# Optimization experiments

Measured on AMD Instinct MI355X. Metric: run time of the kernel, lower is better.

## Reference

```python
import jax, jax.numpy as jnp
import numpy as np

B, T, E = 4, 2048, 1024
H = 16
DH = E // H
SCALE = DH ** -0.5


def setup_inputs() -> dict:
    key = jax.random.key(0)
    ks = jax.random.split(key, 5)
    # small init scale for weights to keep softmax well-conditioned
    return {
        "x": jax.random.normal(ks[0], (B, T, E), dtype=jnp.float32),
        "w_qkv": jax.random.normal(ks[1], (3 * E, E), dtype=jnp.float32) * 0.02,
        "b_qkv": jax.random.normal(ks[2], (3 * E,), dtype=jnp.float32) * 0.02,
        "w_proj": jax.random.normal(ks[3], (E, E), dtype=jnp.float32) * 0.02,
        "b_proj": jax.random.normal(ks[4], (E,), dtype=jnp.float32) * 0.02,
    }


def reference(x, w_qkv, b_qkv, w_proj, b_proj):
    Bs, Ts, Es = x.shape
    # fused qkv projection (torch Linear: y = x W^T + b)
    qkv = x @ w_qkv.T + b_qkv                       # [B,T,3E]
    qkv = qkv.reshape(Bs, Ts, 3, H, DH)
    q, k, v = qkv[:, :, 0], qkv[:, :, 1], qkv[:, :, 2]  # [B,T,H,DH]
    # scores: materialize full TxT matrix per head, as in the original
    scores = jnp.einsum("bthd,bshd->bhts", q, k) * SCALE  # [B,H,T,T]
    causal = jnp.tril(jnp.ones((Ts, Ts), dtype=bool))
    scores = jnp.where(causal[None, None], scores, jnp.float32(-jnp.inf))
    attn = jax.nn.softmax(scores, axis=-1)
    # dropout = 0.0 (eval / deterministic reference)
    out = jnp.einsum("bhts,bshd->bthd", attn, v)    # [B,T,H,DH]
    out = out.reshape(Bs, Ts, Es)
    return out @ w_proj.T + b_proj
```

## Files before the change

### kernel.cpp

```cpp
#include <hip/hip_runtime.h>
#include <hip/hip_bf16.h>

#define B_ 4
#define T_ 2048
#define E_ 1024
#define H_ 16
#define DH_ 64
#define QSCALE_ 0.18033688f

typedef __attribute__((ext_vector_type(8))) short bf16x8;
typedef __attribute__((ext_vector_type(4))) float f32x4;
typedef unsigned int u32;

__device__ inline ushort f2bf(float f) {
    union { float f; unsigned u; } v; v.f = f;
    unsigned r = (v.u + 0x7fffu + ((v.u >> 16) & 1u)) >> 16;
    return (ushort)r;
}

__device__ inline u32 pack2bf(float a, float b) {
    union { float f; u32 u; } ua, ub; ua.f = a; ub.f = b;
    return __builtin_amdgcn_perm(ub.u, ua.u, 0x07060302);
}

__device__ inline void gload16(const ushort* g, ushort* l) {
    __builtin_amdgcn_global_load_lds((const __attribute__((address_space(1))) u32*)g,
                                     (__attribute__((address_space(3))) u32*)l, 16, 0, 0);
}

__global__ void cvt_all(const float* __restrict__ x, const float* __restrict__ wq,
                        const float* __restrict__ wp,
                        ushort* __restrict__ xo, ushort* __restrict__ wqo, ushort* __restrict__ wpo)
{
    const int NX = B_ * T_ * E_ / 4;
    const int NW = 3 * E_ * E_ / 4;
    int i = blockIdx.x * 256 + threadIdx.x;
    const float* s; ushort* d; int off;
    if (i < NX)            { s = x;  d = xo;  off = i; }
    else if (i < NX + NW)  { s = wq; d = wqo; off = i - NX; }
    else                   { s = wp; d = wpo; off = i - NX - NW; }
    float4 f = ((const float4*)s)[off];
    ushort4 u;
    u.x = f2bf(f.x); u.y = f2bf(f.y); u.z = f2bf(f.z); u.w = f2bf(f.w);
    ((ushort4*)d)[off] = u;
}


#define STAGE3(t_) { const int ss_ = (t_) & 3; const int sk_ = (t_) * 32;      \
    gload16(gA0 + sk_, &As[ss_][wave * 512]);                                  \
    gload16(gA1 + sk_, &As[ss_][4096 + wave * 512]);                           \
    gload16(gB0 + sk_, &Bs[ss_][wave * 512]); }

#define GPHASE(t_, vmstr_, DOSTAGE_, ...) do {                                 \
    const int seg_ = (t_) & 3;                                                 \
    bf16x8 afr[4], bfr[4];                                                     \
    _Pragma("unroll") for (int i_ = 0; i_ < 4; i_++)                           \
        afr[i_] = *(const bf16x8*)&As[seg_][(mbase + i_ * 16) * 32 + rofs];    \
    _Pragma("unroll") for (int j_ = 0; j_ < 4; j_++)                           \
        bfr[j_] = *(const bf16x8*)&Bs[seg_][(nbase + j_ * 16) * 32 + rofs];    \
    if (DOSTAGE_) STAGE3((t_) + 3);                                            \
    asm volatile("s_waitcnt " vmstr_ ::: "memory");                            \
    __builtin_amdgcn_s_barrier();                                              \
    asm volatile("s_waitcnt lgkmcnt(0)" ::: "memory");                         \
    __builtin_amdgcn_sched_barrier(0);                                         \
    __builtin_amdgcn_s_setprio(1);                                             \
    __VA_ARGS__                                                                \
    __builtin_amdgcn_s_setprio(0);                                             \
    __builtin_amdgcn_sched_barrier(0);                                         \
    __builtin_amdgcn_s_barrier();                                              \
    __builtin_amdgcn_sched_barrier(0);                                         \
} while (0)

#define MFMA_QKV                                                               \
    if (ct) {                                                                  \
        _Pragma("unroll") for (int i_ = 0; i_ < 4; i_++)                       \
        _Pragma("unroll") for (int j_ = 0; j_ < 4; j_++)                       \
            acc[i_][j_] = __builtin_amdgcn_mfma_f32_16x16x32_bf16(bfr[j_], afr[i_], acc[i_][j_], 0, 0, 0); \
    } else {                                                                   \
        _Pragma("unroll") for (int i_ = 0; i_ < 4; i_++)                       \
        _Pragma("unroll") for (int j_ = 0; j_ < 4; j_++)                       \
            acc[i_][j_] = __builtin_amdgcn_mfma_f32_16x16x32_bf16(afr[i_], bfr[j_], acc[i_][j_], 0, 0, 0); \
    }

#define MFMA_CT                                                                \
    _Pragma("unroll") for (int i_ = 0; i_ < 4; i_++)                           \
    _Pragma("unroll") for (int j_ = 0; j_ < 4; j_++)                           \
        acc[i_][j_] = __builtin_amdgcn_mfma_f32_16x16x32_bf16(bfr[j_], afr[i_], acc[i_][j_], 0, 0, 0);

__global__ __launch_bounds__(512, 2) void gemm_qkv(
    const ushort* __restrict__ Xb, const ushort* __restrict__ Wb,
    const float* __restrict__ bias,
    ushort* __restrict__ Q, ushort* __restrict__ K, ushort* __restrict__ Vt)
{
    __shared__ ushort As[4][256 * 32];
    __shared__ ushort Bs[4][128 * 32];
    const int m0 = blockIdx.x * 256;
    const int n0 = blockIdx.y * 128;
    const int kind = n0 >> 10;
    const int tid  = threadIdx.x;
    const int wave = tid >> 6, lane = tid & 63;
    const int lrow = lane & 15, quad = lane >> 4;
    const int mbase = (wave >> 1) * 64;
    const int nbase = (wave & 1) * 64;
    const int rofs = (lrow >> 1) * 64 + (((((lrow & 1) << 2) | quad) ^ (lrow >> 1)) * 8);
    const int sx  = (lane & 7) ^ (lane >> 3);
    const int sRl = 2 * (lane >> 3) + (sx >> 2);
    const int su  = (sx & 3) * 8;

    const ushort* gA0 = Xb + (size_t)(m0 + wave * 16 + sRl) * 1024 + su;
    const ushort* gA1 = gA0 + (size_t)128 * 1024;
    const ushort* gB0 = Wb + (size_t)(n0 + wave * 16 + sRl) * 1024 + su;

    const int b = m0 >> 11;
    const bool ct = (kind != 2);

    f32x4 acc[4][4];
#pragma unroll
    for (int i = 0; i < 4; i++)
#pragma unroll
        for (int j = 0; j < 4; j++) acc[i][j] = f32x4{0.f, 0.f, 0.f, 0.f};

    STAGE3(0); STAGE3(1); STAGE3(2);
    asm volatile("s_waitcnt vmcnt(6)" ::: "memory");
    __builtin_amdgcn_s_barrier();
    __builtin_amdgcn_sched_barrier(0);

#pragma unroll 4
    for (int t = 0; t < 29; t++) GPHASE(t, "vmcnt(6)", 1, MFMA_QKV);
    GPHASE(29, "vmcnt(3)", 0, MFMA_QKV);
    GPHASE(30, "vmcnt(0)", 0, MFMA_QKV);
    GPHASE(31, "vmcnt(0)", 0, MFMA_QKV);

    if (ct) {
        ushort* dst = (kind == 0) ? Q : K;
        const float scale = (kind == 0) ? QSCALE_ : 1.f;
#pragma unroll
        for (int j = 0; j < 4; j++) {
            int nq = (n0 & 1023) + nbase + j * 16 + quad * 4;
            int h = nq >> 6, d = nq & 63;
            float4 bv = *(const float4*)&bias[n0 + nbase + j * 16 + quad * 4];
            size_t bh = (size_t)(b * H_ + h);
#pragma unroll
            for (int i = 0; i < 4; i++) {
                int t = (m0 + mbase + i * 16 + lrow) & 2047;
                ushort4 o;
                o.x = f2bf((acc[i][j][0] + bv.x) * scale);
                o.y = f2bf((acc[i][j][1] + bv.y) * scale);
                o.z = f2bf((acc[i][j][2] + bv.z) * scale);
                o.w = f2bf((acc[i][j][3] + bv.w) * scale);
                *(ushort4*)&dst[(bh * T_ + t) * DH_ + d] = o;
            }
        }
    } else {
#pragma unroll
        for (int j = 0; j < 4; j++) {
            int nv = (n0 & 1023) + nbase + j * 16 + lrow;
            int h = nv >> 6, d = nv & 63;
            float bv = bias[n0 + nbase + j * 16 + lrow];
            size_t bh = (size_t)(b * H_ + h);
#pragma unroll
            for (int i = 0; i < 4; i++) {
                int t = (m0 + mbase + i * 16 + quad * 4) & 2047;
                ushort4 o;
                o.x = f2bf(acc[i][j][0] + bv);
                o.y = f2bf(acc[i][j][1] + bv);
                o.z = f2bf(acc[i][j][2] + bv);
                o.w = f2bf(acc[i][j][3] + bv);
                *(ushort4*)&Vt[(bh * DH_ + d) * T_ + t] = o;
            }
        }
    }
}

#define LDT_ 76

__global__ __launch_bounds__(256) void flash_attn(
    const ushort* __restrict__ Q, const ushort* __restrict__ K,
    const ushort* __restrict__ Vg,
    ushort* __restrict__ O)
{
    __shared__ ushort Ks[64 * LDT_];
    __shared__ ushort Vt[64 * LDT_];
    __shared__ ushort Ps[128 * LDT_];

    const int qtA = 15 - blockIdx.x;
    const int qtB = blockIdx.x;
    const int bh = blockIdx.y;
    const int tid  = threadIdx.x;
    const int wave = tid >> 6, lane = tid & 63;
    const int lrow = lane & 15, quad = lane >> 4;
    const int sr = tid >> 2, sc = (tid & 3) * 16;

    const ushort* Qbh = Q  + (size_t)bh * T_ * DH_;
    const ushort* Kbh = K  + (size_t)bh * T_ * DH_;
    const ushort* Vbh = Vg + (size_t)bh * DH_ * T_;
    const int b_ = bh >> 4, h_ = bh & 15;

    auto stageQ = [&](int qt, bf16x8 qa[2][2]) {
        int qr = tid >> 1, qc = (tid & 1) * 32;
        const ushort* src = &Qbh[(size_t)(qt * 128 + qr) * DH_ + qc];
#pragma unroll
        for (int i = 0; i < 4; i++)
            *(int4*)&Ps[qr * LDT_ + qc + 8 * i] = *(const int4*)&src[8 * i];
        __syncthreads();
#pragma unroll
        for (int s = 0; s < 2; s++)
#pragma unroll
            for (int h = 0; h < 2; h++)
                qa[s][h] = *(const bf16x8*)&Ps[(s * 64 + wave * 16 + lrow) * LDT_ + h * 32 + quad * 8];
    };

    bf16x8 qaA[2][2], qaB[2][2];
    stageQ(qtA, qaA);
    __syncthreads();
    stageQ(qtB, qaB);

    auto run = [&](const bf16x8 (&qa)[2][2], int qt) {
        const int lastkt = 2 * qt + 1;

        int4 kr0 = *(const int4*)&Kbh[(size_t)sr * DH_ + sc];
        int4 kr1 = *(const int4*)&Kbh[(size_t)sr * DH_ + sc + 8];
        int4 vr0 = *(const int4*)&Vbh[(size_t)sr * T_ + sc];
        int4 vr1 = *(const int4*)&Vbh[(size_t)sr * T_ + sc + 8];

        float ls[2] = {0.f, 0.f};
        f32x4 accO[2][4];
#pragma unroll
        for (int s = 0; s < 2; s++)
#pragma unroll
            for (int j = 0; j < 4; j++) accO[s][j] = f32x4{0.f, 0.f, 0.f, 0.f};

        for (int kt = 0; kt <= lastkt; ++kt) {
            __syncthreads();
            *(int4*)&Ks[sr * LDT_ + sc]     = kr0;
            *(int4*)&Ks[sr * LDT_ + sc + 8] = kr1;
            *(int4*)&Vt[sr * LDT_ + sc]     = vr0;
            *(int4*)&Vt[sr * LDT_ + sc + 8] = vr1;
            __syncthreads();
            if (kt < lastkt) {
                kr0 = *(const int4*)&Kbh[(size_t)((kt + 1) * 64 + sr) * DH_ + sc];
                kr1 = *(const int4*)&Kbh[(size_t)((kt + 1) * 64 + sr) * DH_ + sc + 8];
                vr0 = *(const int4*)&Vbh[(size_t)sr * T_ + (kt + 1) * 64 + sc];
                vr1 = *(const int4*)&Vbh[(size_t)sr * T_ + (kt + 1) * 64 + sc + 8];
            }

            bf16x8 kb0[4], kb1[4];
#pragma unroll
            for (int j = 0; j < 4; j++) {
                kb0[j] = *(const bf16x8*)&Ks[(j * 16 + lrow) * LDT_ + quad * 8];
                kb1[j] = *(const bf16x8*)&Ks[(j * 16 + lrow) * LDT_ + 32 + quad * 8];
            }

            const bool do0 = (kt != lastkt);
#pragma unroll
            for (int s = 0; s < 2; s++) {
                if (s == 0 && !do0) continue;
                f32x4 st[4];
#pragma unroll
                for (int j = 0; j < 4; j++) {
                    f32x4 sj = f32x4{0.f, 0.f, 0.f, 0.f};
                    sj = __builtin_amdgcn_mfma_f32_16x16x32_bf16(kb0[j], qa[s][0], sj, 0, 0, 0);
                    sj = __builtin_amdgcn_mfma_f32_16x16x32_bf16(kb1[j], qa[s][1], sj, 0, 0, 0);
                    st[j] = sj;
                }
                if (kt == 2 * qt + s) {
                    const int qrow = qt * 128 + s * 64 + wave * 16 + lrow;
                    const int keyb = kt * 64 + quad * 4;
#pragma unroll
                    for (int j = 0; j < 4; j++)
#pragma unroll
                        for (int r = 0; r < 4; r++)
                            if (keyb + j * 16 + r > qrow) st[j][r] = -1e30f;
                }
                float lp = 0.f;
#pragma unroll
                for (int j = 0; j < 4; j++)
#pragma unroll
                    for (int r = 0; r < 4; r++) {
                        float p = __builtin_amdgcn_exp2f(st[j][r]);
                        st[j][r] = p;
                        lp += p;
                    }
                ls[s] += lp;
                ushort* prow = &Ps[(s * 64 + wave * 16 + lrow) * LDT_ + quad * 4];
#pragma unroll
                for (int j = 0; j < 4; j++) {
                    *(u32*)&prow[j * 16]     = pack2bf(st[j][0], st[j][1]);
                    *(u32*)&prow[j * 16 + 2] = pack2bf(st[j][2], st[j][3]);
                }
            }

            bf16x8 vb0[4], vb1[4];
#pragma unroll
            for (int j = 0; j < 4; j++) {
                vb0[j] = *(const bf16x8*)&Vt[(j * 16 + lrow) * LDT_ + quad * 8];
                vb1[j] = *(const bf16x8*)&Vt[(j * 16 + lrow) * LDT_ + 32 + quad * 8];
            }
#pragma unroll
            for (int s = 0; s < 2; s++) {
                if (s == 0 && !do0) continue;
                bf16x8 pa0 = *(const bf16x8*)&Ps[(s * 64 + wave * 16 + lrow) * LDT_ + quad * 8];
                bf16x8 pa1 = *(const bf16x8*)&Ps[(s * 64 + wave * 16 + lrow) * LDT_ + 32 + quad * 8];
#pragma unroll
                for (int jd = 0; jd < 4; jd++) {
                    accO[s][jd] = __builtin_amdgcn_mfma_f32_16x16x32_bf16(pa0, vb0[jd], accO[s][jd], 0, 0, 0);
                    accO[s][jd] = __builtin_amdgcn_mfma_f32_16x16x32_bf16(pa1, vb1[jd], accO[s][jd], 0, 0, 0);
                }
            }
        }

#pragma unroll
        for (int s = 0; s < 2; s++) {
            ls[s] += __shfl_xor(ls[s], 16, 64);
            ls[s] += __shfl_xor(ls[s], 32, 64);
        }
#pragma unroll
        for (int s = 0; s < 2; s++) {
#pragma unroll
            for (int r = 0; r < 4; r++) {
                float lv = __shfl(ls[s], quad * 4 + r, 64);
                float inv = 1.f / lv;
                int t = qt * 128 + s * 64 + wave * 16 + quad * 4 + r;
#pragma unroll
                for (int jd = 0; jd < 4; jd++) {
                    int d = jd * 16 + lrow;
                    O[((size_t)(b_ * T_ + t)) * E_ + h_ * DH_ + d] = f2bf(accO[s][jd][r] * inv);
                }
            }
        }
    };

    run(qaA, qtA);
    run(qaB, qtB);
}

__global__ __launch_bounds__(512, 2) void gemm_proj(
    const ushort* __restrict__ Ob, const ushort* __restrict__ Wb,
    const float* __restrict__ bias, float* __restrict__ out)
{
    __shared__ ushort As[4][256 * 32];
    __shared__ ushort Bs[4][128 * 32];
    const int m0 = blockIdx.x * 256;
    const int n0 = blockIdx.y * 128;
    const int tid  = threadIdx.x;
    const int wave = tid >> 6, lane = tid & 63;
    const int lrow = lane & 15, quad = lane >> 4;
    const int mbase = (wave >> 1) * 64;
    const int nbase = (wave & 1) * 64;
    const int rofs = (lrow >> 1) * 64 + (((((lrow & 1) << 2) | quad) ^ (lrow >> 1)) * 8);
    const int sx  = (lane & 7) ^ (lane >> 3);
    const int sRl = 2 * (lane >> 3) + (sx >> 2);
    const int su  = (sx & 3) * 8;

    const ushort* gA0 = Ob + (size_t)(m0 + wave * 16 + sRl) * 1024 + su;
    const ushort* gA1 = gA0 + (size_t)128 * 1024;
    const ushort* gB0 = Wb + (size_t)(n0 + wave * 16 + sRl) * 1024 + su;

    f32x4 acc[4][4];
#pragma unroll
    for (int i = 0; i < 4; i++)
#pragma unroll
        for (int j = 0; j < 4; j++) acc[i][j] = f32x4{0.f, 0.f, 0.f, 0.f};

    STAGE3(0); STAGE3(1); STAGE3(2);
    asm volatile("s_waitcnt vmcnt(6)" ::: "memory");
    __builtin_amdgcn_s_barrier();
    __builtin_amdgcn_sched_barrier(0);

#pragma unroll 4
    for (int t = 0; t < 29; t++) GPHASE(t, "vmcnt(6)", 1, MFMA_CT);
    GPHASE(29, "vmcnt(3)", 0, MFMA_CT);
    GPHASE(30, "vmcnt(0)", 0, MFMA_CT);
    GPHASE(31, "vmcnt(0)", 0, MFMA_CT);

#pragma unroll
    for (int j = 0; j < 4; j++) {
        int n = n0 + nbase + j * 16 + quad * 4;
        float4 bv = *(const float4*)&bias[n];
#pragma unroll
        for (int i = 0; i < 4; i++) {
            int m = m0 + mbase + i * 16 + lrow;
            float4 o;
            o.x = acc[i][j][0] + bv.x;
            o.y = acc[i][j][1] + bv.y;
            o.z = acc[i][j][2] + bv.z;
            o.w = acc[i][j][3] + bv.w;
            *(float4*)&out[(size_t)m * 1024 + n] = o;
        }
    }
}

extern "C" void kernel_launch(void* const* d_in, const int* in_sizes, int n_in,
                              void* d_out, int out_size, void* d_ws, size_t ws_size,
                              hipStream_t stream) {
    const float* x      = (const float*)d_in[0];
    const float* w_qkv  = (const float*)d_in[1];
    const float* b_qkv  = (const float*)d_in[2];
    const float* w_proj = (const float*)d_in[3];
    const float* b_proj = (const float*)d_in[4];
    float* out = (float*)d_out;

    char* ws = (char*)d_ws;
    ushort* Xb     = (ushort*)ws; ws += (size_t)B_ * T_ * E_ * 2;
    ushort* Wqkvb  = (ushort*)ws; ws += (size_t)3 * E_ * E_ * 2;
    ushort* Wprojb = (ushort*)ws; ws += (size_t)E_ * E_ * 2;
    ushort* Qb     = (ushort*)ws; ws += (size_t)B_ * H_ * T_ * DH_ * 2;
    ushort* Kb     = (ushort*)ws; ws += (size_t)B_ * H_ * T_ * DH_ * 2;
    ushort* Vtb    = (ushort*)ws; ws += (size_t)B_ * H_ * T_ * DH_ * 2;
    ushort* Ob     = (ushort*)ws; ws += (size_t)B_ * T_ * E_ * 2;

    int ntot = (B_ * T_ * E_ + 3 * E_ * E_ + E_ * E_) / 4;
    cvt_all<<<ntot / 256, 256, 0, stream>>>(x, w_qkv, w_proj, Xb, Wqkvb, Wprojb);

    gemm_qkv<<<dim3(32, 24), 512, 0, stream>>>(Xb, Wqkvb, b_qkv, Qb, Kb, Vtb);
    flash_attn<<<dim3(8, 64), 256, 0, stream>>>(Qb, Kb, Vtb, Ob);
    gemm_proj<<<dim3(32, 8), 512, 0, stream>>>(Ob, Wprojb, b_proj, out);
}
```

Measured before the change: 251.6 us.

## Use 4-wave GEMM blocks with 128x64 warp tiles and 3-stage LDS ring

```diff
diff --git a/kernel.cpp b/kernel.cpp
--- a/kernel.cpp
+++ b/kernel.cpp
@@ -46,19 +46,21 @@
 }
 
 
-#define STAGE3(t_) { const int ss_ = (t_) & 3; const int sk_ = (t_) * 32;      \
-    gload16(gA0 + sk_, &As[ss_][wave * 512]);                                  \
-    gload16(gA1 + sk_, &As[ss_][4096 + wave * 512]);                           \
-    gload16(gB0 + sk_, &Bs[ss_][wave * 512]); }
-
-#define GPHASE(t_, vmstr_, DOSTAGE_, ...) do {                                 \
-    const int seg_ = (t_) & 3;                                                 \
-    bf16x8 afr[4], bfr[4];                                                     \
-    _Pragma("unroll") for (int i_ = 0; i_ < 4; i_++)                           \
-        afr[i_] = *(const bf16x8*)&As[seg_][(mbase + i_ * 16) * 32 + rofs];    \
+#define STAGE6(ss_, t_) { const int sk_ = (t_) * 32;                           \
+    gload16(gA0 + sk_,             &As[ss_][(wave * 4 + 0) * 512]);            \
+    gload16(gA0 + 16 * 1024 + sk_, &As[ss_][(wave * 4 + 1) * 512]);            \
+    gload16(gA0 + 32 * 1024 + sk_, &As[ss_][(wave * 4 + 2) * 512]);            \
+    gload16(gA0 + 48 * 1024 + sk_, &As[ss_][(wave * 4 + 3) * 512]);            \
+    gload16(gB0 + sk_,             &Bs[ss_][(wave * 2 + 0) * 512]);            \
+    gload16(gB0 + 16 * 1024 + sk_, &Bs[ss_][(wave * 2 + 1) * 512]); }
+
+#define GPHASE(segC_, segS_, t_, vmstr_, DOSTAGE_, ...) do {                   \
+    bf16x8 afr[8], bfr[4];                                                     \
+    _Pragma("unroll") for (int i_ = 0; i_ < 8; i_++)                           \
+        afr[i_] = *(const bf16x8*)&As[segC_][(mbase + i_ * 16) * 32 + rofs];   \
     _Pragma("unroll") for (int j_ = 0; j_ < 4; j_++)                           \
-        bfr[j_] = *(const bf16x8*)&Bs[seg_][(nbase + j_ * 16) * 32 + rofs];    \
-    if (DOSTAGE_) STAGE3((t_) + 3);                                            \
+        bfr[j_] = *(const bf16x8*)&Bs[segC_][(nbase + j_ * 16) * 32 + rofs];   \
+    if (DOSTAGE_) STAGE6(segS_, (t_) + 2);                                     \
     asm volatile("s_waitcnt " vmstr_ ::: "memory");                            \
     __builtin_amdgcn_s_barrier();                                              \
     asm volatile("s_waitcnt lgkmcnt(0)" ::: "memory");                         \
@@ -73,63 +75,67 @@
 
 #define MFMA_QKV                                                               \
     if (ct) {                                                                  \
-        _Pragma("unroll") for (int i_ = 0; i_ < 4; i_++)                       \
+        _Pragma("unroll") for (int i_ = 0; i_ < 8; i_++)                       \
         _Pragma("unroll") for (int j_ = 0; j_ < 4; j_++)                       \
             acc[i_][j_] = __builtin_amdgcn_mfma_f32_16x16x32_bf16(bfr[j_], afr[i_], acc[i_][j_], 0, 0, 0); \
     } else {                                                                   \
-        _Pragma("unroll") for (int i_ = 0; i_ < 4; i_++)                       \
+        _Pragma("unroll") for (int i_ = 0; i_ < 8; i_++)                       \
         _Pragma("unroll") for (int j_ = 0; j_ < 4; j_++)                       \
             acc[i_][j_] = __builtin_amdgcn_mfma_f32_16x16x32_bf16(afr[i_], bfr[j_], acc[i_][j_], 0, 0, 0); \
     }
 
 #define MFMA_CT                                                                \
-    _Pragma("unroll") for (int i_ = 0; i_ < 4; i_++)                           \
+    _Pragma("unroll") for (int i_ = 0; i_ < 8; i_++)                           \
     _Pragma("unroll") for (int j_ = 0; j_ < 4; j_++)                           \
         acc[i_][j_] = __builtin_amdgcn_mfma_f32_16x16x32_bf16(bfr[j_], afr[i_], acc[i_][j_], 0, 0, 0);
 
-__global__ __launch_bounds__(512, 2) void gemm_qkv(
+#define GEMM_MAIN(MFMABLK_)                                                    \
+    STAGE6(0, 0); STAGE6(1, 1);                                                \
+    asm volatile("s_waitcnt vmcnt(6)" ::: "memory");                           \
+    __builtin_amdgcn_s_barrier();                                              \
+    __builtin_amdgcn_sched_barrier(0);                                         \
+    _Pragma("unroll 1")                                                        \
+    for (int t = 0; t < 30; t += 3) {                                          \
+        GPHASE(0, 2, t + 0, "vmcnt(6)", 1, MFMABLK_);                          \
+        GPHASE(1, 0, t + 1, "vmcnt(6)", 1, MFMABLK_);                          \
+        GPHASE(2, 1, t + 2, "vmcnt(6)", 1, MFMABLK_);                          \
+    }                                                                          \
+    GPHASE(0, 0, 30, "vmcnt(0)", 0, MFMABLK_);                                 \
+    GPHASE(1, 0, 31, "vmcnt(0)", 0, MFMABLK_);
+
+__global__ __launch_bounds__(256, 2) void gemm_qkv(
     const ushort* __restrict__ Xb, const ushort* __restrict__ Wb,
     const float* __restrict__ bias,
     ushort* __restrict__ Q, ushort* __restrict__ K, ushort* __restrict__ Vt)
 {
-    __shared__ ushort As[4][256 * 32];
-    __shared__ ushort Bs[4][128 * 32];
+    __shared__ ushort As[3][256 * 32];
+    __shared__ ushort Bs[3][128 * 32];
     const int m0 = blockIdx.x * 256;
     const int n0 = blockIdx.y * 128;
     const int kind = n0 >> 10;
     const int tid  = threadIdx.x;
     const int wave = tid >> 6, lane = tid & 63;
     const int lrow = lane & 15, quad = lane >> 4;
-    const int mbase = (wave >> 1) * 64;
+    const int mbase = (wave >> 1) * 128;
     const int nbase = (wave & 1) * 64;
     const int rofs = (lrow >> 1) * 64 + (((((lrow & 1) << 2) | quad) ^ (lrow >> 1)) * 8);
     const int sx  = (lane & 7) ^ (lane >> 3);
     const int sRl = 2 * (lane >> 3) + (sx >> 2);
     const int su  = (sx & 3) * 8;
 
-    const ushort* gA0 = Xb + (size_t)(m0 + wave * 16 + sRl) * 1024 + su;
-    const ushort* gA1 = gA0 + (size_t)128 * 1024;
-    const ushort* gB0 = Wb + (size_t)(n0 + wave * 16 + sRl) * 1024 + su;
+    const ushort* gA0 = Xb + (size_t)(m0 + wave * 64 + sRl) * 1024 + su;
+    const ushort* gB0 = Wb + (size_t)(n0 + wave * 32 + sRl) * 1024 + su;
 
     const int b = m0 >> 11;
     const bool ct = (kind != 2);
 
-    f32x4 acc[4][4];
-#pragma unroll
-    for (int i = 0; i < 4; i++)
+    f32x4 acc[8][4];
+#pragma unroll
+    for (int i = 0; i < 8; i++)
 #pragma unroll
         for (int j = 0; j < 4; j++) acc[i][j] = f32x4{0.f, 0.f, 0.f, 0.f};
 
-    STAGE3(0); STAGE3(1); STAGE3(2);
-    asm volatile("s_waitcnt vmcnt(6)" ::: "memory");
-    __builtin_amdgcn_s_barrier();
-    __builtin_amdgcn_sched_barrier(0);
-
-#pragma unroll 4
-    for (int t = 0; t < 29; t++) GPHASE(t, "vmcnt(6)", 1, MFMA_QKV);
-    GPHASE(29, "vmcnt(3)", 0, MFMA_QKV);
-    GPHASE(30, "vmcnt(0)", 0, MFMA_QKV);
-    GPHASE(31, "vmcnt(0)", 0, MFMA_QKV);
+    GEMM_MAIN(MFMA_QKV)
 
     if (ct) {
         ushort* dst = (kind == 0) ? Q : K;
@@ -141,7 +147,7 @@
             float4 bv = *(const float4*)&bias[n0 + nbase + j * 16 + quad * 4];
             size_t bh = (size_t)(b * H_ + h);
 #pragma unroll
-            for (int i = 0; i < 4; i++) {
+            for (int i = 0; i < 8; i++) {
                 int t = (m0 + mbase + i * 16 + lrow) & 2047;
                 ushort4 o;
                 o.x = f2bf((acc[i][j][0] + bv.x) * scale);
@@ -159,7 +165,7 @@
             float bv = bias[n0 + nbase + j * 16 + lrow];
             size_t bh = (size_t)(b * H_ + h);
 #pragma unroll
-            for (int i = 0; i < 4; i++) {
+            for (int i = 0; i < 8; i++) {
                 int t = (m0 + mbase + i * 16 + quad * 4) & 2047;
                 ushort4 o;
                 o.x = f2bf(acc[i][j][0] + bv);
@@ -334,51 +340,41 @@
     run(qaB, qtB);
 }
 
-__global__ __launch_bounds__(512, 2) void gemm_proj(
+__global__ __launch_bounds__(256, 2) void gemm_proj(
     const ushort* __restrict__ Ob, const ushort* __restrict__ Wb,
     const float* __restrict__ bias, float* __restrict__ out)
 {
-    __shared__ ushort As[4][256 * 32];
-    __shared__ ushort Bs[4][128 * 32];
+    __shared__ ushort As[3][256 * 32];
+    __shared__ ushort Bs[3][128 * 32];
     const int m0 = blockIdx.x * 256;
     const int n0 = blockIdx.y * 128;
     const int tid  = threadIdx.x;
     const int wave = tid >> 6, lane = tid & 63;
     const int lrow = lane & 15, quad = lane >> 4;
-    const int mbase = (wave >> 1) * 64;
+    const int mbase = (wave >> 1) * 128;
     const int nbase = (wave & 1) * 64;
     const int rofs = (lrow >> 1) * 64 + (((((lrow & 1) << 2) | quad) ^ (lrow >> 1)) * 8);
     const int sx  = (lane & 7) ^ (lane >> 3);
     const int sRl = 2 * (lane >> 3) + (sx >> 2);
     const int su  = (sx & 3) * 8;
 
-    const ushort* gA0 = Ob + (size_t)(m0 + wave * 16 + sRl) * 1024 + su;
-    const ushort* gA1 = gA0 + (size_t)128 * 1024;
-    const ushort* gB0 = Wb + (size_t)(n0 + wave * 16 + sRl) * 1024 + su;
-
-    f32x4 acc[4][4];
-#pragma unroll
-    for (int i = 0; i < 4; i++)
+    const ushort* gA0 = Ob + (size_t)(m0 + wave * 64 + sRl) * 1024 + su;
+    const ushort* gB0 = Wb + (size_t)(n0 + wave * 32 + sRl) * 1024 + su;
+
+    f32x4 acc[8][4];
+#pragma unroll
+    for (int i = 0; i < 8; i++)
 #pragma unroll
         for (int j = 0; j < 4; j++) acc[i][j] = f32x4{0.f, 0.f, 0.f, 0.f};
 
-    STAGE3(0); STAGE3(1); STAGE3(2);
-    asm volatile("s_waitcnt vmcnt(6)" ::: "memory");
-    __builtin_amdgcn_s_barrier();
-    __builtin_amdgcn_sched_barrier(0);
-
-#pragma unroll 4
-    for (int t = 0; t < 29; t++) GPHASE(t, "vmcnt(6)", 1, MFMA_CT);
-    GPHASE(29, "vmcnt(3)", 0, MFMA_CT);
-    GPHASE(30, "vmcnt(0)", 0, MFMA_CT);
-    GPHASE(31, "vmcnt(0)", 0, MFMA_CT);
+    GEMM_MAIN(MFMA_CT)
 
 #pragma unroll
     for (int j = 0; j < 4; j++) {
         int n = n0 + nbase + j * 16 + quad * 4;
         float4 bv = *(const float4*)&bias[n];
 #pragma unroll
-        for (int i = 0; i < 4; i++) {
+        for (int i = 0; i < 8; i++) {
             int m = m0 + mbase + i * 16 + lrow;
             float4 o;
             o.x = acc[i][j][0] + bv.x;
@@ -412,7 +408,7 @@
     int ntot = (B_ * T_ * E_ + 3 * E_ * E_ + E_ * E_) / 4;
     cvt_all<<<ntot / 256, 256, 0, stream>>>(x, w_qkv, w_proj, Xb, Wqkvb, Wprojb);
 
-    gemm_qkv<<<dim3(32, 24), 512, 0, stream>>>(Xb, Wqkvb, b_qkv, Qb, Kb, Vtb);
+    gemm_qkv<<<dim3(32, 24), 256, 0, stream>>>(Xb, Wqkvb, b_qkv, Qb, Kb, Vtb);
     flash_attn<<<dim3(8, 64), 256, 0, stream>>>(Qb, Kb, Vtb, Ob);
-    gemm_proj<<<dim3(32, 8), 512, 0, stream>>>(Ob, Wprojb, b_proj, out);
-}
+    gemm_proj<<<dim3(32, 8), 256, 0, stream>>>(Ob, Wprojb, b_proj, out);
+}
```

Result: slower. 642.0 us (+155.1%).
